# Performance work log

Measured on AMD Instinct MI355X. Metric: run time of the kernel, lower is better.

Reference implementation:

```python
import jax, jax.numpy as jnp
import numpy as np
from jax import lax

K = 3  # kernel_size
PAD = 1
STRIDE = 1
DIL = 1


def setup_inputs() -> dict:
    key = jax.random.key(0)
    k1, k2 = jax.random.split(key)
    x = jax.random.normal(k1, (32, 256, 56, 56), dtype=jnp.float32)
    weights = jax.random.normal(k2, (256, 256, K * K), dtype=jnp.float32) * 0.05
    return {"x": x, "weights": weights}


def reference(x, weights):
    B, C, H, W = x.shape
    O = weights.shape[0]
    # weights stored as [O, C, k*k] -> standard OIHW conv kernel
    w = weights.reshape(O, C, K, K)
    # Dense conv replaces the per-(channel, filter) matmul loop over im2col windows.
    y = lax.conv_general_dilated(
        x, w,
        window_strides=(STRIDE, STRIDE),
        padding=[(PAD, PAD), (PAD, PAD)],
        rhs_dilation=(DIL, DIL),
        dimension_numbers=("NCHW", "OIHW", "NCHW"),
    )  # [B, O, Hout, Wout]
    Hout, Wout = y.shape[2], y.shape[3]
    # Faithful to original: results buffer is laid out [O, B, Hout, Wout]
    # (out-channel-major blocks of batch) then reinterpreted as [B, O, Hout, Wout].
    result = jnp.transpose(y, (1, 0, 2, 3)).reshape(B, O, Hout, Wout)
    return result
```

## Files before the change

kernel.cpp:

```cpp
#include <hip/hip_runtime.h>
#include <hip/hip_bf16.h>

using s8v   = __attribute__((ext_vector_type(8))) short;
using f32x4 = __attribute__((ext_vector_type(4))) float;

#define N_TOT 100352
#define WT_ELEMS 589824
#define PLANE_ELEMS 861184
#define XT_ELEMS 27557888
#define WS_NEED  56295424

#define BAR() asm volatile("s_barrier" ::: "memory")
#define GATE(T) do { if ((T) < 33) asm volatile("s_waitcnt vmcnt(8)" ::: "memory"); \
                     else          asm volatile("s_waitcnt vmcnt(0)" ::: "memory"); } while (0)

__device__ __forceinline__ unsigned short f2bf(float f) {
    unsigned int u = __float_as_uint(f);
    unsigned int r = (u + 0x7FFF + ((u >> 16) & 1)) >> 16;
    return (unsigned short)r;
}

__device__ __forceinline__ void gl_lds16(const void* g, void* l) {
    __builtin_amdgcn_global_load_lds(
        (const __attribute__((address_space(1))) unsigned int*)g,
        (__attribute__((address_space(3))) unsigned int*)l, 16, 0, 0);
}

__global__ void prep_w(const float* __restrict__ w, unsigned short* __restrict__ wt) {
    int u = blockIdx.x * 256 + threadIdx.x;
    int kt = u >> 11;
    int r  = u & 2047;
    int o  = r >> 3;
    int s  = r & 7;
    int ksub  = s ^ (o & 7);
    int kstep = kt * 2 + (ksub >> 2);
    int cb = kstep / 9, tap = kstep - cb * 9;
    int c0 = cb * 32 + (ksub & 3) * 8;
    const float* src = w + ((size_t)(o * 256 + c0)) * 9 + tap;
    unsigned int p[4];
    #pragma unroll
    for (int q = 0; q < 4; ++q) {
        float f0 = src[(2 * q) * 9];
        float f1 = src[(2 * q + 1) * 9];
        p[q] = (unsigned)f2bf(f0) | ((unsigned)f2bf(f1) << 16);
    }
    *(uint4*)(wt + (size_t)u * 8) = *(uint4*)p;
}

__global__ void prep_x(const float* __restrict__ x, unsigned short* __restrict__ xt) {
    int b  = blockIdx.x / 58;
    int hp = blockIdx.x % 58;
    int tid = threadIdx.x;
    uint4 zero = {0u, 0u, 0u, 0u};
    size_t rowbase = (size_t)(b * 58 + hp) * 58;
    if (hp == 0 || hp == 57) {
        for (int i = tid; i < 1856; i += 256) {
            int cg = i / 58, wp = i - cg * 58;
            *(uint4*)(xt + ((size_t)cg * PLANE_ELEMS + (rowbase + wp) * 8)) = zero;
        }
        return;
    }
    int h = hp - 1;
    int wave = tid >> 6, lane = tid & 63;
    for (int cg = wave; cg < 32; cg += 4) {
        unsigned short* outp = xt + (size_t)cg * PLANE_ELEMS + rowbase * 8;
        if (lane < 56) {
            const float* src = x + ((size_t)(b * 256 + cg * 8) * 3136 + h * 56 + lane);
            unsigned int p[4];
            #pragma unroll
            for (int q = 0; q < 4; ++q) {
                float f0 = src[(size_t)(2 * q) * 3136];
                float f1 = src[(size_t)(2 * q + 1) * 3136];
                p[q] = (unsigned)f2bf(f0) | ((unsigned)f2bf(f1) << 16);
            }
            *(uint4*)(outp + (size_t)(lane + 1) * 8) = *(uint4*)p;
        } else if (lane == 56) {
            *(uint4*)outp = zero;
        } else if (lane == 57) {
            *(uint4*)(outp + 57 * 8) = zero;
        }
    }
}

__global__ __launch_bounds__(512, 2) void gemm8(const unsigned short* __restrict__ wt,
                                                const unsigned short* __restrict__ xt,
                                                float* __restrict__ out) {
    extern __shared__ char lds[];
    int bx = blockIdx.x;
    int nt = (bx & 7) * 49 + (bx >> 3);
    int tid  = threadIdx.x;
    int w    = tid >> 6, lane = tid & 63;
    int l16  = lane & 15, quad = lane >> 4;
    int wm   = w >> 2,   wn   = w & 3;
    int lane16 = lane * 16;

    int s0 = w * 2, s1 = w * 2 + 1;
    int adst0 = ((s0 >> 3) * 128 + (s0 & 7) * 8) * 128;
    int adst1 = ((s1 >> 3) * 128 + (s1 & 7) * 8) * 128;
    int bp0 = ((s0 >> 2) * 64 + (s0 & 3) * 8);
    int bp1 = ((s1 >> 2) * 64 + (s1 & 3) * 8);
    int bdst0 = bp0 * 128;
    int bdst1 = bp1 * 128;
    int ksub  = (lane & 7) ^ (lane >> 3);
    int ksl   = ksub >> 2;
    int c2off = (ksub & 3) * PLANE_ELEMS;
    int pix[2][2];
    #pragma unroll
    for (int it = 0; it < 2; ++it)
        #pragma unroll
        for (int h = 0; h < 2; ++h) {
            int n = nt * 256 + (it ? bp1 : bp0) + h * 32 + (lane >> 3);
            int b = n / 3136; int rr = n - b * 3136;
            int hh = rr / 56; int ww = rr - hh * 56;
            pix[it][h] = ((b * 58 + hh) * 58 + ww) * 8;
        }
    int pix00 = pix[0][0], pix01 = pix[0][1], pix10 = pix[1][0], pix11 = pix[1][1];

    int swz = (quad ^ (l16 & 7)) << 4;
    int aK0 = wm * 16384 + l16 * 128 + swz;
    int aK1 = aK0 ^ 64;
    int bK0 = 32768 + wn * 8192 + l16 * 128 + swz;
    int bK1 = bK0 ^ 64;

    auto SA = [&](char* buf, const char* srcTile, int roff) {
        gl_lds16(srcTile + adst0 + roff + lane16, buf + adst0 + roff);
        gl_lds16(srcTile + adst1 + roff + lane16, buf + adst1 + roff);
    };
    auto SB = [&](char* buf, int bo0, int bo1, int h) {
        int bsel = (ksl ? bo1 : bo0) + c2off;
        gl_lds16(xt + (size_t)(unsigned)(bsel + (h ? pix01 : pix00)),
                 buf + 32768 + bdst0 + h * 4096);
        gl_lds16(xt + (size_t)(unsigned)(bsel + (h ? pix11 : pix10)),
                 buf + 32768 + bdst1 + h * 4096);
    };
    auto BO = [&](int ks) {
        int cb = ks / 9, tap = ks - cb * 9;
        return cb * 4 * PLANE_ELEMS + ((tap / 3) * 58 + (tap - (tap / 3) * 3)) * 8;
    };

    f32x4 acc[8][4] = {};
    s8v aE0[4], aE1[4], aO0[4], aO1[4];
    s8v bE0[2], bE1[2], bO0[2], bO1[2];

    #define MFMA_Q(MH, NH, A0, A1, B0, B1)                                         \
        __builtin_amdgcn_s_setprio(1);                                             \
        _Pragma("unroll")                                                          \
        for (int f = 0; f < 4; ++f) {                                              \
            _Pragma("unroll")                                                      \
            for (int g = 0; g < 2; ++g)                                            \
                acc[(MH)*4+f][(NH)*2+g] = __builtin_amdgcn_mfma_f32_16x16x32_bf16( \
                    A0[f], B0[g], acc[(MH)*4+f][(NH)*2+g], 0, 0, 0);               \
        }                                                                          \
        _Pragma("unroll")                                                          \
        for (int f = 0; f < 4; ++f) {                                              \
            _Pragma("unroll")                                                      \
            for (int g = 0; g < 2; ++g)                                            \
                acc[(MH)*4+f][(NH)*2+g] = __builtin_amdgcn_mfma_f32_16x16x32_bf16( \
                    A1[f], B1[g], acc[(MH)*4+f][(NH)*2+g], 0, 0, 0);               \
        }                                                                          \
        __builtin_amdgcn_s_setprio(0);

    SA(lds, (const char*)wt, 0);
    SA(lds, (const char*)wt, 8192);
    SB(lds, BO(0), BO(1), 0);
    SB(lds, BO(0), BO(1), 1);
    SA(lds + 65536, (const char*)wt + 32768, 0);
    SB(lds + 65536, BO(2), BO(3), 0);
    SB(lds + 65536, BO(2), BO(3), 1);
    asm volatile("s_waitcnt vmcnt(6)" ::: "memory");
    BAR();
    #pragma unroll
    for (int f = 0; f < 4; ++f) {
        aE0[f] = *(const s8v*)(lds + aK0 + f * 2048);
        aE1[f] = *(const s8v*)(lds + aK1 + f * 2048);
    }
    #pragma unroll
    for (int g = 0; g < 2; ++g) {
        bE0[g] = *(const s8v*)(lds + bK0 + g * 2048);
        bE1[g] = *(const s8v*)(lds + bK1 + g * 2048);
    }

    #pragma unroll 1
    for (int t = 0; t < 36; ++t) {
        char* bufc = lds + (t & 1) * 65536;
        char* bufo = lds + ((t & 1) ^ 1) * 65536;
        const char* wA1 = (const char*)wt + (size_t)(t + 1) * 32768;
        const char* wA0 = (const char*)wt + (size_t)(t + 2) * 32768;
        int kk  = 2 * (t + 2);
        int bo0 = BO(kk);
        int bo1 = BO(kk + 1);

        BAR();
        #pragma unroll
        for (int g = 0; g < 2; ++g) {
            bO0[g] = *(const s8v*)(bufc + bK0 + 4096 + g * 2048);
            bO1[g] = *(const s8v*)(bufc + bK1 + 4096 + g * 2048);
        }
        if (t < 35) SA(bufo, wA1, 8192);
        MFMA_Q(0, 0, aE0, aE1, bE0, bE1)
        GATE(t);

        BAR();
        #pragma unroll
        for (int f = 0; f < 4; ++f)
            aO0[f] = *(const s8v*)(bufc + aK0 + 8192 + f * 2048);
        if (t < 34) SA(bufc, wA0, 0);
        MFMA_Q(0, 1, aE0, aE1, bO0, bO1)
        GATE(t);

        BAR();
        #pragma unroll
        for (int f = 0; f < 4; ++f)
            aO1[f] = *(const s8v*)(bufc + aK1 + 8192 + f * 2048);
        if (t < 35) {
            #pragma unroll
            for (int f = 0; f < 4; ++f)
                aE0[f] = *(const s8v*)(bufo + aK0 + f * 2048);
        }
        if (t < 34) SB(bufc, bo0, bo1, 0);
        MFMA_Q(1, 0, aO0, aO1, bE0, bE1)
        GATE(t);

        BAR();
        if (t < 35) {
            #pragma unroll
            for (int f = 0; f < 4; ++f)
                aE1[f] = *(const s8v*)(bufo + aK1 + f * 2048);
            #pragma unroll
            for (int g = 0; g < 2; ++g) {
                bE0[g] = *(const s8v*)(bufo + bK0 + g * 2048);
                bE1[g] = *(const s8v*)(bufo + bK1 + g * 2048);
            }
        }
        if (t < 34) SB(bufc, bo0, bo1, 1);
        MFMA_Q(1, 1, aO0, aO1, bO0, bO1)
        GATE(t);
    }

    float* op = out + (size_t)(wm * 128 + quad * 4) * N_TOT + nt * 256 + wn * 64 + l16;
    #pragma unroll
    for (int f = 0; f < 8; ++f)
        #pragma unroll
        for (int rr = 0; rr < 4; ++rr) {
            float* orow = op + (size_t)(f * 16 + rr) * N_TOT;
            #pragma unroll
            for (int g = 0; g < 4; ++g)
                orow[g * 16] = acc[f][g][rr];
        }
}

__global__ void conv_naive(const float* __restrict__ x, const float* __restrict__ wq,
                           float* __restrict__ out) {
    int f = blockIdx.x * 256 + threadIdx.x;
    int o = f / N_TOT;
    int n = f - o * N_TOT;
    int b = n / 3136; int r = n - b * 3136; int h = r / 56; int w = r - h * 56;
    const float* xb = x + (size_t)b * 256 * 3136;
    const float* wo = wq + o * 2304;
    float acc = 0.f;
    for (int c = 0; c < 256; ++c) {
        const float* xc = xb + c * 3136;
        const float* wc = wo + c * 9;
        #pragma unroll
        for (int dh = 0; dh < 3; ++dh) {
            int ih = h + dh - 1;
            if (ih < 0 || ih >= 56) continue;
            const float* xr = xc + ih * 56;
            #pragma unroll
            for (int dw = 0; dw < 3; ++dw) {
                int iw = w + dw - 1;
                if (iw >= 0 && iw < 56) acc += xr[iw] * wc[dh * 3 + dw];
            }
        }
    }
    out[f] = acc;
}

extern "C" void kernel_launch(void* const* d_in, const int* in_sizes, int n_in,
                              void* d_out, int out_size, void* d_ws, size_t ws_size,
                              hipStream_t stream) {
    const float* x = (const float*)d_in[0];
    const float* w = (const float*)d_in[1];
    float* out = (float*)d_out;
    if (ws_size >= (size_t)WS_NEED) {
        unsigned short* wt = (unsigned short*)d_ws;
        unsigned short* xt = wt + WT_ELEMS;
        static int attr_done = 0;
        if (!attr_done) {
            hipFuncSetAttribute((const void*)gemm8,
                                hipFuncAttributeMaxDynamicSharedMemorySize, 131072);
            attr_done = 1;
        }
        prep_w<<<288, 256, 0, stream>>>(w, wt);
        prep_x<<<32 * 58, 256, 0, stream>>>(x, xt);
        gemm8<<<392, 512, 131072, stream>>>(wt, xt, out);
    } else {
        conv_naive<<<N_TOT, 256, 0, stream>>>(x, w, out);
    }
}
```

Before: 321.2 us.

## Switch padded input layout from channel-group planes to NHWC pixel-major

The bf16 padded input buffer changes from 32 separate channel-group planes (8 channels each) to a layout where each padded pixel stores all 256 channels contiguously. The prep kernel now transposes through an LDS tile so it can write 16-byte chunks per pixel, and the GEMM's B-tile address math is switched to byte offsets with a pixel stride of 512 bytes. This is meant to give the implicit-GEMM B loads better locality, since the 32-channel k-slice per pixel becomes 64 contiguous bytes instead of 16-byte pieces spread across distant planes. The cost is a more complex prep transpose with two barriers per pass, and the prep kernel's global reads are now per-channel scalar loads.

```diff
diff --git a/kernel.cpp b/kernel.cpp
--- a/kernel.cpp
+++ b/kernel.cpp
@@ -6,7 +6,6 @@
 
 #define N_TOT 100352
 #define WT_ELEMS 589824
-#define PLANE_ELEMS 861184
 #define XT_ELEMS 27557888
 #define WS_NEED  56295424
 
@@ -52,34 +51,34 @@
     int hp = blockIdx.x % 58;
     int tid = threadIdx.x;
     uint4 zero = {0u, 0u, 0u, 0u};
-    size_t rowbase = (size_t)(b * 58 + hp) * 58;
+    size_t rowbase = (size_t)(b * 58 + hp) * 58 * 256;
     if (hp == 0 || hp == 57) {
-        for (int i = tid; i < 1856; i += 256) {
-            int cg = i / 58, wp = i - cg * 58;
-            *(uint4*)(xt + ((size_t)cg * PLANE_ELEMS + (rowbase + wp) * 8)) = zero;
-        }
+        for (int i = tid; i < 1856; i += 256)
+            *(uint4*)(xt + rowbase + (size_t)i * 8) = zero;
         return;
     }
     int h = hp - 1;
-    int wave = tid >> 6, lane = tid & 63;
-    for (int cg = wave; cg < 32; cg += 4) {
-        unsigned short* outp = xt + (size_t)cg * PLANE_ELEMS + rowbase * 8;
-        if (lane < 56) {
-            const float* src = x + ((size_t)(b * 256 + cg * 8) * 3136 + h * 56 + lane);
-            unsigned int p[4];
-            #pragma unroll
-            for (int q = 0; q < 4; ++q) {
-                float f0 = src[(size_t)(2 * q) * 3136];
-                float f1 = src[(size_t)(2 * q + 1) * 3136];
-                p[q] = (unsigned)f2bf(f0) | ((unsigned)f2bf(f1) << 16);
-            }
-            *(uint4*)(outp + (size_t)(lane + 1) * 8) = *(uint4*)p;
-        } else if (lane == 56) {
-            *(uint4*)outp = zero;
-        } else if (lane == 57) {
-            *(uint4*)(outp + 57 * 8) = zero;
-        }
-    }
+    __shared__ unsigned short T[56][72];
+    int wv = tid >> 6, lane = tid & 63;
+    int p   = tid >> 2, seg = tid & 3;
+    #pragma unroll 1
+    for (int pass = 0; pass < 4; ++pass) {
+        #pragma unroll
+        for (int j = 0; j < 16; ++j) {
+            int c = pass * 64 + wv * 16 + j;
+            if (lane < 56)
+                T[lane][wv * 16 + j] = f2bf(x[((size_t)(b * 256 + c)) * 3136 + h * 56 + lane]);
+        }
+        __syncthreads();
+        if (p < 56) {
+            unsigned short* dst = xt + rowbase + (size_t)(p + 1) * 256 + pass * 64 + seg * 16;
+            *(uint4*)dst       = *(uint4*)&T[p][seg * 16];
+            *(uint4*)(dst + 8) = *(uint4*)&T[p][seg * 16 + 8];
+        }
+        __syncthreads();
+    }
+    if (tid < 32)       *(uint4*)(xt + rowbase + (size_t)tid * 8) = zero;
+    else if (tid < 64)  *(uint4*)(xt + rowbase + (size_t)57 * 256 + (size_t)(tid - 32) * 8) = zero;
 }
 
 __global__ __launch_bounds__(512, 2) void gemm8(const unsigned short* __restrict__ wt,
@@ -103,7 +102,7 @@
     int bdst1 = bp1 * 128;
     int ksub  = (lane & 7) ^ (lane >> 3);
     int ksl   = ksub >> 2;
-    int c2off = (ksub & 3) * PLANE_ELEMS;
+    int c2off = (ksub & 3) * 16;
     int pix[2][2];
     #pragma unroll
     for (int it = 0; it < 2; ++it)
@@ -112,7 +111,7 @@
             int n = nt * 256 + (it ? bp1 : bp0) + h * 32 + (lane >> 3);
             int b = n / 3136; int rr = n - b * 3136;
             int hh = rr / 56; int ww = rr - hh * 56;
-            pix[it][h] = ((b * 58 + hh) * 58 + ww) * 8;
+            pix[it][h] = ((b * 58 + hh) * 58 + ww) * 512;
         }
     int pix00 = pix[0][0], pix01 = pix[0][1], pix10 = pix[1][0], pix11 = pix[1][1];
 
@@ -122,20 +121,21 @@
     int bK0 = 32768 + wn * 8192 + l16 * 128 + swz;
     int bK1 = bK0 ^ 64;
 
+    const char* xtB = (const char*)xt;
     auto SA = [&](char* buf, const char* srcTile, int roff) {
         gl_lds16(srcTile + adst0 + roff + lane16, buf + adst0 + roff);
         gl_lds16(srcTile + adst1 + roff + lane16, buf + adst1 + roff);
     };
     auto SB = [&](char* buf, int bo0, int bo1, int h) {
         int bsel = (ksl ? bo1 : bo0) + c2off;
-        gl_lds16(xt + (size_t)(unsigned)(bsel + (h ? pix01 : pix00)),
+        gl_lds16(xtB + (size_t)(unsigned)(bsel + (h ? pix01 : pix00)),
                  buf + 32768 + bdst0 + h * 4096);
-        gl_lds16(xt + (size_t)(unsigned)(bsel + (h ? pix11 : pix10)),
+        gl_lds16(xtB + (size_t)(unsigned)(bsel + (h ? pix11 : pix10)),
                  buf + 32768 + bdst1 + h * 4096);
     };
     auto BO = [&](int ks) {
         int cb = ks / 9, tap = ks - cb * 9;
-        return cb * 4 * PLANE_ELEMS + ((tap / 3) * 58 + (tap - (tap / 3) * 3)) * 8;
+        return ((tap / 3) * 58 + (tap - (tap / 3) * 3)) * 512 + cb * 64;
     };
 
     f32x4 acc[8][4] = {};
```

New measurement: 319.0 us. No clear change (-0.7%).
